# Kernel tuning notes

Hardware: AMD Instinct MI355X
Metric: run time of the kernel (lower is better)

The kernel has to match this reference:

```python
import jax, jax.numpy as jnp
import numpy as np

B, T, I, H, O, R = 128, 1024, 64, 512, 32, 2
TAU = 0.2
NOISE_STD = 0.05


def setup_inputs() -> dict:
    key = jax.random.key(0)
    ks = jax.random.split(key, 12)
    def xavier(k, shape):
        fan_in, fan_out = shape[1], shape[0]
        lim = float(np.sqrt(6.0 / (fan_in + fan_out)))
        return jax.random.uniform(k, shape, jnp.float32, -lim, lim)
    return {
        "u": jax.random.normal(ks[0], (B, T, I), jnp.float32),
        "x0": jax.random.normal(ks[1], (B, H), jnp.float32),
        "noise": jax.random.normal(ks[2], (T, B, H), jnp.float32),
        "Win_w": xavier(ks[3], (H, I)),
        "Win_b": jnp.zeros((H,), jnp.float32),
        "Wout_w": xavier(ks[4], (O, H)),
        "Wout_b": jax.random.normal(ks[5], (O,), jnp.float32) * 0.01,
        "M_rnn": xavier(ks[6], (H, R)),
        "N_rnn": xavier(ks[7], (H, R)),
        "L_tb": xavier(ks[8], (H, R)),
        "M_tb": xavier(ks[9], (H, R)),
        "N_tb": xavier(ks[10], (H, R)),
    }


def reference(u, x0, noise, Win_w, Win_b, Wout_w, Wout_b,
              M_rnn, N_rnn, L_tb, M_tb, N_tb):
    # mode='cont', form='rate', adv=False
    Hdim = x0.shape[1]
    scale_rnn = 1.0 / Hdim
    scale_tb = 1.0 / (Hdim * Hdim)
    # precompute input projection for all timesteps: [T, B, H]
    inp_t = jnp.transpose(jnp.einsum('bti,hi->bth', u, Win_w) + Win_b, (1, 0, 2))

    def step(x, xs):
        ip, nz = xs                                # [B,H] each
        r = jnp.tanh(x)                            # rate form
        rec_rnn = (r @ N_rnn) @ M_rnn.T * scale_rnn
        rec_tb = ((r @ M_tb) * (r @ N_tb)) @ L_tb.T * scale_tb
        rec_x = rec_rnn + rec_tb + ip
        x_new = x + NOISE_STD * nz + TAU * (-x + rec_x)
        return x_new, x_new

    x_final, traj_t = jax.lax.scan(step, x0, (inp_t, noise))
    traj = jnp.transpose(traj_t, (1, 0, 2))        # [B,T,H]
    output = jnp.tanh(traj) @ Wout_w.T + Wout_b    # [B,T,O]
    return output, x_final, traj
```

## Files before the change

### kernel.cpp

```cpp
#include <hip/hip_runtime.h>

constexpr int kB = 128;
constexpr int kT = 1024;
constexpr int kI = 64;
constexpr int kH = 512;
constexpr int kO = 32;
constexpr float kTau = 0.2f;
constexpr float kNoise = 0.05f;

__device__ __forceinline__ float fast_tanh(float x) {
    float e = __expf(2.0f * x);
    return 1.0f - 2.0f * __builtin_amdgcn_rcpf(e + 1.0f);
}

#define BARW() do { asm volatile("s_waitcnt lgkmcnt(0)" ::: "memory"); \
                    __builtin_amdgcn_s_barrier();                      \
                    asm volatile("" ::: "memory"); } while (0)

template <int CTRL, int RMASK>
__device__ __forceinline__ float dpp_add(float s) {
    return s + __int_as_float(__builtin_amdgcn_update_dpp(
        0, __float_as_int(s), CTRL, RMASK, 0xf, true));
}
__device__ __forceinline__ float wave_sum64_lane63(float s) {
    s = dpp_add<0x111, 0xf>(s);
    s = dpp_add<0x112, 0xf>(s);
    s = dpp_add<0x114, 0xf>(s);
    s = dpp_add<0x118, 0xf>(s);
    s = dpp_add<0x142, 0xa>(s);
    s = dpp_add<0x143, 0xc>(s);
    return s;
}

__global__ __launch_bounds__(512, 2) void scan_kernel(
    const float* __restrict__ u, const float* __restrict__ x0,
    const float* __restrict__ noise, const float* __restrict__ Win_w,
    const float* __restrict__ Win_b, const float* __restrict__ M_rnn,
    const float* __restrict__ N_rnn, const float* __restrict__ L_tb,
    const float* __restrict__ M_tb, const float* __restrict__ N_tb,
    float* __restrict__ traj, float* __restrict__ xfin)
{
    const int b    = blockIdx.x;
    const int h    = threadIdx.x;
    const int wid  = h >> 6;
    const int lane = h & 63;

    __shared__ float red[6 * kH];
    __shared__ __align__(16) float res[8];

    float W[kI];
    #pragma unroll
    for (int i = 0; i < kI; i += 4) {
        float4 w = *(const float4*)&Win_w[h * kI + i];
        W[i] = w.x; W[i + 1] = w.y; W[i + 2] = w.z; W[i + 3] = w.w;
    }
    #pragma unroll
    for (int i = 0; i < kI; ++i) asm volatile("" : "+v"(W[i]));

    const float wb  = Win_b[h];
    const float Nr0 = N_rnn[h * 2], Nr1 = N_rnn[h * 2 + 1];
    const float Mt0 = M_tb[h * 2],  Mt1 = M_tb[h * 2 + 1];
    const float Nt0 = N_tb[h * 2],  Nt1 = N_tb[h * 2 + 1];
    const float sc_rnn = 1.0f / (float)kH;
    const float sc_tb  = 1.0f / ((float)kH * (float)kH);
    const float Mr0 = M_rnn[h * 2] * sc_rnn, Mr1 = M_rnn[h * 2 + 1] * sc_rnn;
    const float Lt0 = L_tb[h * 2] * sc_tb,   Lt1 = L_tb[h * 2 + 1] * sc_tb;

    float x = x0[b * kH + h];

    const float* up  = u + (size_t)b * kT * kI;
    const float* nzp = noise + (size_t)b * kH + h;
    float* tp = traj + (size_t)b * kT * kH + h;

    float4 ur[16];
    {
        const float4* u4 = (const float4*)up;
        #pragma unroll
        for (int i = 0; i < 16; ++i) ur[i] = u4[i];
    }
    float nzA = nzp[0];
    float nzB = nzp[(size_t)kB * kH];

    auto step = [&](int t, float& nzC) {
        float r = fast_tanh(x);
        red[0 * kH + h] = r * Nr0;
        red[1 * kH + h] = r * Nr1;
        red[2 * kH + h] = r * Mt0;
        red[3 * kH + h] = r * Mt1;
        red[4 * kH + h] = r * Nt0;
        red[5 * kH + h] = r * Nt1;
        BARW();
        if (wid < 6) {
            const float* c = red + wid * kH + lane;
            float s0 = c[0]   + c[64];
            float s1 = c[128] + c[192];
            float s2 = c[256] + c[320];
            float s3 = c[384] + c[448];
            float s  = (s0 + s1) + (s2 + s3);
            s = wave_sum64_lane63(s);
            if (lane == 63) res[wid] = s;
        }
        BARW();
        float4 r4 = *(const float4*)&res[0];
        float2 r2 = *(const float2*)&res[4];
        float ip = wb;
        #pragma unroll
        for (int i = 0; i < 16; ++i) {
            ip += ur[i].x * W[4 * i]     + ur[i].y * W[4 * i + 1]
                + ur[i].z * W[4 * i + 2] + ur[i].w * W[4 * i + 3];
        }
        {
            int tn = (t + 1 < kT) ? t + 1 : kT - 1;
            const float4* u4 = (const float4*)(up + (size_t)tn * kI);
            #pragma unroll
            for (int i = 0; i < 16; ++i) ur[i] = u4[i];
        }
        float rec = r4.x * Mr0 + r4.y * Mr1
                  + (r4.z * r2.x) * Lt0 + (r4.w * r2.y) * Lt1 + ip;
        x = (1.0f - kTau) * x + kNoise * nzC + kTau * rec;
        tp[(size_t)t * kH] = x;
        int t2 = (t + 2 < kT) ? t + 2 : kT - 1;
        nzC = nzp[(size_t)t2 * kB * kH];
    };

    for (int t = 0; t < kT; t += 2) {
        step(t, nzA);
        step(t + 1, nzB);
    }
    xfin[b * kH + h] = x;
}

constexpr int R_BLK = 256;
constexpr int H_CHK = 32;
constexpr int AS_LD = 260;

__global__ __launch_bounds__(256, 2) void out_kernel(
    const float* __restrict__ traj, const float* __restrict__ Wout_w,
    const float* __restrict__ Wout_b, float* __restrict__ out)
{
    __shared__ float As[H_CHK][AS_LD];
    __shared__ float Ws[H_CHK][36];

    const int tid = threadIdx.x;
    const size_t row0 = (size_t)blockIdx.x * R_BLK;
    const int og = tid & 3;
    const int rg = tid >> 2;

    float acc[4][8];
    #pragma unroll
    for (int k = 0; k < 4; ++k)
        #pragma unroll
        for (int j = 0; j < 8; ++j) acc[k][j] = 0.f;

    const int lr = tid >> 3;
    const int lc4 = tid & 7;
    const int wo = tid >> 3;
    const int wc = (tid & 7) * 4;

    for (int ch = 0; ch < 16; ++ch) {
        const int hc = ch * H_CHK;
        float4 a[8];
        #pragma unroll
        for (int j = 0; j < 8; ++j) {
            const int r = j * 32 + lr;
            a[j] = *(const float4*)&traj[(row0 + r) * kH + hc + lc4 * 4];
        }
        float4 w = *(const float4*)&Wout_w[wo * kH + hc + wc];
        __syncthreads();
        #pragma unroll
        for (int j = 0; j < 8; ++j) {
            const int r = j * 32 + lr;
            As[lc4 * 4 + 0][r] = fast_tanh(a[j].x);
            As[lc4 * 4 + 1][r] = fast_tanh(a[j].y);
            As[lc4 * 4 + 2][r] = fast_tanh(a[j].z);
            As[lc4 * 4 + 3][r] = fast_tanh(a[j].w);
        }
        Ws[wc + 0][wo] = w.x;
        Ws[wc + 1][wo] = w.y;
        Ws[wc + 2][wo] = w.z;
        Ws[wc + 3][wo] = w.w;
        __syncthreads();
        #pragma unroll
        for (int hh = 0; hh < H_CHK; ++hh) {
            float4 av = *(const float4*)&As[hh][rg * 4];
            float4 w0 = *(const float4*)&Ws[hh][og * 8];
            float4 w1 = *(const float4*)&Ws[hh][og * 8 + 4];
            const float av4[4] = {av.x, av.y, av.z, av.w};
            const float wv[8]  = {w0.x, w0.y, w0.z, w0.w,
                                  w1.x, w1.y, w1.z, w1.w};
            #pragma unroll
            for (int k = 0; k < 4; ++k)
                #pragma unroll
                for (int j = 0; j < 8; ++j)
                    acc[k][j] += av4[k] * wv[j];
        }
    }

    #pragma unroll
    for (int k = 0; k < 4; ++k) {
        const size_t row = row0 + rg * 4 + k;
        float4 v0, v1;
        v0.x = acc[k][0] + Wout_b[og * 8 + 0];
        v0.y = acc[k][1] + Wout_b[og * 8 + 1];
        v0.z = acc[k][2] + Wout_b[og * 8 + 2];
        v0.w = acc[k][3] + Wout_b[og * 8 + 3];
        v1.x = acc[k][4] + Wout_b[og * 8 + 4];
        v1.y = acc[k][5] + Wout_b[og * 8 + 5];
        v1.z = acc[k][6] + Wout_b[og * 8 + 6];
        v1.w = acc[k][7] + Wout_b[og * 8 + 7];
        *(float4*)&out[row * kO + og * 8]     = v0;
        *(float4*)&out[row * kO + og * 8 + 4] = v1;
    }
}

extern "C" void kernel_launch(void* const* d_in, const int* in_sizes, int n_in,
                              void* d_out, int out_size, void* d_ws, size_t ws_size,
                              hipStream_t stream) {
    const float* u      = (const float*)d_in[0];
    const float* x0     = (const float*)d_in[1];
    const float* noise  = (const float*)d_in[2];
    const float* Win_w  = (const float*)d_in[3];
    const float* Win_b  = (const float*)d_in[4];
    const float* Wout_w = (const float*)d_in[5];
    const float* Wout_b = (const float*)d_in[6];
    const float* M_rnn  = (const float*)d_in[7];
    const float* N_rnn  = (const float*)d_in[8];
    const float* L_tb   = (const float*)d_in[9];
    const float* M_tb   = (const float*)d_in[10];
    const float* N_tb   = (const float*)d_in[11];

    float* out  = (float*)d_out;
    float* xfin = out + (size_t)kB * kT * kO;
    float* traj = xfin + (size_t)kB * kH;

    scan_kernel<<<dim3(kB), dim3(kH), 0, stream>>>(
        u, x0, noise, Win_w, Win_b, M_rnn, N_rnn, L_tb, M_tb, N_tb, traj, xfin);
    out_kernel<<<dim3((kB * kT) / R_BLK), dim3(256), 0, stream>>>(
        traj, Wout_w, Wout_b, out);
}
```

Measured before the change: 1.466 ms.

## Precompute input projection and noise, shuffle-based scan reduction, double-buffer output GEMM

Adds a separate parallel kernel that computes tau-scaled input projection plus noise for every (b,t) and stores it into the traj buffer. The serial scan then reads that precomputed term in place of the 64-wide dot product and the noise load each step. The scan's cross-thread reduction now uses DPP reductions per wave plus a small shared-memory stage, rather than a 6x512 shared array. The output kernel gains double-buffered LDS with register prefetch and a remapped block order. This adds an extra full pass writing and reading traj in exchange for a shorter serial critical path.

```diff
diff --git a/kernel.cpp b/kernel.cpp
--- a/kernel.cpp
+++ b/kernel.cpp
@@ -22,20 +22,53 @@
     return s + __int_as_float(__builtin_amdgcn_update_dpp(
         0, __float_as_int(s), CTRL, RMASK, 0xf, true));
 }
-__device__ __forceinline__ float wave_sum64_lane63(float s) {
-    s = dpp_add<0x111, 0xf>(s);
-    s = dpp_add<0x112, 0xf>(s);
-    s = dpp_add<0x114, 0xf>(s);
-    s = dpp_add<0x118, 0xf>(s);
-    s = dpp_add<0x142, 0xa>(s);
-    s = dpp_add<0x143, 0xc>(s);
-    return s;
+
+constexpr int ROWS_PB = 64;
+
+__global__ __launch_bounds__(256, 2) void inp_kernel(
+    const float* __restrict__ u, const float* __restrict__ Win_w,
+    const float* __restrict__ Win_b, const float* __restrict__ noise,
+    float* __restrict__ traj)
+{
+    const int tid = threadIdx.x;
+    const int h2 = tid * 2;
+    const size_t row0 = (size_t)blockIdx.x * ROWS_PB;
+
+    float W0[kI], W1[kI];
+    #pragma unroll
+    for (int i = 0; i < kI; i += 4) {
+        float4 a = *(const float4*)&Win_w[(size_t)h2 * kI + i];
+        float4 c = *(const float4*)&Win_w[(size_t)(h2 + 1) * kI + i];
+        W0[i] = a.x * kTau; W0[i + 1] = a.y * kTau;
+        W0[i + 2] = a.z * kTau; W0[i + 3] = a.w * kTau;
+        W1[i] = c.x * kTau; W1[i + 1] = c.y * kTau;
+        W1[i + 2] = c.z * kTau; W1[i + 3] = c.w * kTau;
+    }
+    const float twb0 = Win_b[h2] * kTau;
+    const float twb1 = Win_b[h2 + 1] * kTau;
+
+    for (int r = 0; r < ROWS_PB; ++r) {
+        const size_t row = row0 + r;
+        const float* ur = u + row * kI;
+        float ip0 = twb0, ip1 = twb1;
+        #pragma unroll
+        for (int i = 0; i < kI; ++i) {
+            float ui = ur[i];
+            ip0 += ui * W0[i];
+            ip1 += ui * W1[i];
+        }
+        const int t = (int)(row & (kT - 1));
+        const int b = (int)(row >> 10);
+        float2 nz = *(const float2*)&noise[((size_t)t * kB + b) * kH + h2];
+        float2 c;
+        c.x = ip0 + kNoise * nz.x;
+        c.y = ip1 + kNoise * nz.y;
+        *(float2*)&traj[row * kH + h2] = c;
+    }
 }
 
 __global__ __launch_bounds__(512, 2) void scan_kernel(
-    const float* __restrict__ u, const float* __restrict__ x0,
-    const float* __restrict__ noise, const float* __restrict__ Win_w,
-    const float* __restrict__ Win_b, const float* __restrict__ M_rnn,
+    const float* __restrict__ x0, const float* __restrict__ M_rnn,
     const float* __restrict__ N_rnn, const float* __restrict__ L_tb,
     const float* __restrict__ M_tb, const float* __restrict__ N_tb,
     float* __restrict__ traj, float* __restrict__ xfin)
@@ -45,87 +78,69 @@
     const int wid  = h >> 6;
     const int lane = h & 63;
 
-    __shared__ float red[6 * kH];
+    __shared__ float pp[64];
     __shared__ __align__(16) float res[8];
 
-    float W[kI];
-    #pragma unroll
-    for (int i = 0; i < kI; i += 4) {
-        float4 w = *(const float4*)&Win_w[h * kI + i];
-        W[i] = w.x; W[i + 1] = w.y; W[i + 2] = w.z; W[i + 3] = w.w;
-    }
-    #pragma unroll
-    for (int i = 0; i < kI; ++i) asm volatile("" : "+v"(W[i]));
-
-    const float wb  = Win_b[h];
     const float Nr0 = N_rnn[h * 2], Nr1 = N_rnn[h * 2 + 1];
     const float Mt0 = M_tb[h * 2],  Mt1 = M_tb[h * 2 + 1];
     const float Nt0 = N_tb[h * 2],  Nt1 = N_tb[h * 2 + 1];
-    const float sc_rnn = 1.0f / (float)kH;
-    const float sc_tb  = 1.0f / ((float)kH * (float)kH);
-    const float Mr0 = M_rnn[h * 2] * sc_rnn, Mr1 = M_rnn[h * 2 + 1] * sc_rnn;
-    const float Lt0 = L_tb[h * 2] * sc_tb,   Lt1 = L_tb[h * 2 + 1] * sc_tb;
+    const float sr = kTau / (float)kH;
+    const float st = kTau / ((float)kH * (float)kH);
+    const float tMr0 = M_rnn[h * 2] * sr, tMr1 = M_rnn[h * 2 + 1] * sr;
+    const float tLt0 = L_tb[h * 2] * st,  tLt1 = L_tb[h * 2 + 1] * st;
 
     float x = x0[b * kH + h];
-
-    const float* up  = u + (size_t)b * kT * kI;
-    const float* nzp = noise + (size_t)b * kH + h;
     float* tp = traj + (size_t)b * kT * kH + h;
 
-    float4 ur[16];
-    {
-        const float4* u4 = (const float4*)up;
-        #pragma unroll
-        for (int i = 0; i < 16; ++i) ur[i] = u4[i];
-    }
-    float nzA = nzp[0];
-    float nzB = nzp[(size_t)kB * kH];
-
-    auto step = [&](int t, float& nzC) {
+    float cA = tp[0];
+    float cB = tp[kH];
+
+    auto step = [&](int t, float& c) {
         float r = fast_tanh(x);
-        red[0 * kH + h] = r * Nr0;
-        red[1 * kH + h] = r * Nr1;
-        red[2 * kH + h] = r * Mt0;
-        red[3 * kH + h] = r * Mt1;
-        red[4 * kH + h] = r * Nt0;
-        red[5 * kH + h] = r * Nt1;
-        BARW();
-        if (wid < 6) {
-            const float* c = red + wid * kH + lane;
-            float s0 = c[0]   + c[64];
-            float s1 = c[128] + c[192];
-            float s2 = c[256] + c[320];
-            float s3 = c[384] + c[448];
-            float s  = (s0 + s1) + (s2 + s3);
-            s = wave_sum64_lane63(s);
-            if (lane == 63) res[wid] = s;
+        float s0 = r * Nr0, s1 = r * Nr1;
+        float s2 = r * Mt0, s3 = r * Mt1;
+        float s4 = r * Nt0, s5 = r * Nt1;
+        #define STAGE(CTRL, MASK)                                   \
+            s0 = dpp_add<CTRL, MASK>(s0); s1 = dpp_add<CTRL, MASK>(s1); \
+            s2 = dpp_add<CTRL, MASK>(s2); s3 = dpp_add<CTRL, MASK>(s3); \
+            s4 = dpp_add<CTRL, MASK>(s4); s5 = dpp_add<CTRL, MASK>(s5);
+        STAGE(0x111, 0xf)
+        STAGE(0x112, 0xf)
+        STAGE(0x114, 0xf)
+        STAGE(0x118, 0xf)
+        STAGE(0x142, 0xa)
+        STAGE(0x143, 0xc)
+        #undef STAGE
+        if (lane == 63) {
+            pp[0 * 8 + wid] = s0;
+            pp[1 * 8 + wid] = s1;
+            pp[2 * 8 + wid] = s2;
+            pp[3 * 8 + wid] = s3;
+            pp[4 * 8 + wid] = s4;
+            pp[5 * 8 + wid] = s5;
+        }
+        BARW();
+        if (wid == 0) {
+            float v = pp[lane];
+            v = dpp_add<0x111, 0xf>(v);
+            v = dpp_add<0x112, 0xf>(v);
+            v = dpp_add<0x114, 0xf>(v);
+            if ((lane & 7) == 0 && lane < 48) res[lane >> 3] = v;
         }
         BARW();
         float4 r4 = *(const float4*)&res[0];
         float2 r2 = *(const float2*)&res[4];
-        float ip = wb;
-        #pragma unroll
-        for (int i = 0; i < 16; ++i) {
-            ip += ur[i].x * W[4 * i]     + ur[i].y * W[4 * i + 1]
-                + ur[i].z * W[4 * i + 2] + ur[i].w * W[4 * i + 3];
-        }
-        {
-            int tn = (t + 1 < kT) ? t + 1 : kT - 1;
-            const float4* u4 = (const float4*)(up + (size_t)tn * kI);
-            #pragma unroll
-            for (int i = 0; i < 16; ++i) ur[i] = u4[i];
-        }
-        float rec = r4.x * Mr0 + r4.y * Mr1
-                  + (r4.z * r2.x) * Lt0 + (r4.w * r2.y) * Lt1 + ip;
-        x = (1.0f - kTau) * x + kNoise * nzC + kTau * rec;
+        float rr = r4.x * tMr0 + r4.y * tMr1
+                 + (r4.z * r2.x) * tLt0 + (r4.w * r2.y) * tLt1;
+        x = (1.0f - kTau) * x + rr + c;
         tp[(size_t)t * kH] = x;
-        int t2 = (t + 2 < kT) ? t + 2 : kT - 1;
-        nzC = nzp[(size_t)t2 * kB * kH];
+        int t2 = (t + 2) & (kT - 1);
+        c = tp[(size_t)t2 * kH];
     };
 
     for (int t = 0; t < kT; t += 2) {
-        step(t, nzA);
-        step(t + 1, nzB);
+        step(t, cA);
+        step(t + 1, cB);
     }
     xfin[b * kH + h] = x;
 }
@@ -138,13 +153,18 @@
     const float* __restrict__ traj, const float* __restrict__ Wout_w,
     const float* __restrict__ Wout_b, float* __restrict__ out)
 {
-    __shared__ float As[H_CHK][AS_LD];
-    __shared__ float Ws[H_CHK][36];
+    __shared__ float As[2][H_CHK][AS_LD];
+    __shared__ float Ws[2][H_CHK][36];
 
     const int tid = threadIdx.x;
-    const size_t row0 = (size_t)blockIdx.x * R_BLK;
+    const int g = blockIdx.x;
+    const int l = (g & 7) * 4 + ((g >> 3) & 3) + ((g >> 5) << 5);
+    const size_t row0 = (size_t)l * R_BLK;
+
     const int og = tid & 3;
     const int rg = tid >> 2;
+    const int lr = tid >> 3, lc4 = tid & 7;
+    const int wo = tid >> 3, wc = (tid & 7) * 4;
 
     float acc[4][8];
     #pragma unroll
@@ -152,39 +172,41 @@
         #pragma unroll
         for (int j = 0; j < 8; ++j) acc[k][j] = 0.f;
 
-    const int lr = tid >> 3;
-    const int lc4 = tid & 7;
-    const int wo = tid >> 3;
-    const int wc = (tid & 7) * 4;
+    float4 a[8];
+    float4 w;
+    #pragma unroll
+    for (int j = 0; j < 8; ++j)
+        a[j] = *(const float4*)&traj[(row0 + j * 32 + lr) * kH + lc4 * 4];
+    w = *(const float4*)&Wout_w[(size_t)wo * kH + wc];
 
     for (int ch = 0; ch < 16; ++ch) {
-        const int hc = ch * H_CHK;
-        float4 a[8];
+        const int p = ch & 1;
         #pragma unroll
         for (int j = 0; j < 8; ++j) {
-            const int r = j * 32 + lr;
-            a[j] = *(const float4*)&traj[(row0 + r) * kH + hc + lc4 * 4];
-        }
-        float4 w = *(const float4*)&Wout_w[wo * kH + hc + wc];
-        __syncthreads();
-        #pragma unroll
-        for (int j = 0; j < 8; ++j) {
-            const int r = j * 32 + lr;
-            As[lc4 * 4 + 0][r] = fast_tanh(a[j].x);
-            As[lc4 * 4 + 1][r] = fast_tanh(a[j].y);
-            As[lc4 * 4 + 2][r] = fast_tanh(a[j].z);
-            As[lc4 * 4 + 3][r] = fast_tanh(a[j].w);
-        }
-        Ws[wc + 0][wo] = w.x;
-        Ws[wc + 1][wo] = w.y;
-        Ws[wc + 2][wo] = w.z;
-        Ws[wc + 3][wo] = w.w;
-        __syncthreads();
+            const int rr = j * 32 + lr;
+            As[p][lc4 * 4 + 0][rr] = fast_tanh(a[j].x);
+            As[p][lc4 * 4 + 1][rr] = fast_tanh(a[j].y);
+            As[p][lc4 * 4 + 2][rr] = fast_tanh(a[j].z);
+            As[p][lc4 * 4 + 3][rr] = fast_tanh(a[j].w);
+        }
+        Ws[p][wc + 0][wo] = w.x;
+        Ws[p][wc + 1][wo] = w.y;
+        Ws[p][wc + 2][wo] = w.z;
+        Ws[p][wc + 3][wo] = w.w;
+        BARW();
+        if (ch < 15) {
+            const int hc = (ch + 1) * H_CHK;
+            #pragma unroll
+            for (int j = 0; j < 8; ++j)
+                a[j] = *(const float4*)
+                    &traj[(row0 + j * 32 + lr) * kH + hc + lc4 * 4];
+            w = *(const float4*)&Wout_w[(size_t)wo * kH + hc + wc];
+        }
         #pragma unroll
         for (int hh = 0; hh < H_CHK; ++hh) {
-            float4 av = *(const float4*)&As[hh][rg * 4];
-            float4 w0 = *(const float4*)&Ws[hh][og * 8];
-            float4 w1 = *(const float4*)&Ws[hh][og * 8 + 4];
+            float4 av = *(const float4*)&As[p][hh][rg * 4];
+            float4 w0 = *(const float4*)&Ws[p][hh][og * 8];
+            float4 w1 = *(const float4*)&Ws[p][hh][og * 8 + 4];
             const float av4[4] = {av.x, av.y, av.z, av.w};
             const float wv[8]  = {w0.x, w0.y, w0.z, w0.w,
                                   w1.x, w1.y, w1.z, w1.w};
@@ -194,6 +216,7 @@
                 for (int j = 0; j < 8; ++j)
                     acc[k][j] += av4[k] * wv[j];
         }
+        BARW();
     }
 
     #pragma unroll
@@ -233,8 +256,10 @@
     float* xfin = out + (size_t)kB * kT * kO;
     float* traj = xfin + (size_t)kB * kH;
 
+    inp_kernel<<<dim3((kB * kT) / ROWS_PB), dim3(256), 0, stream>>>(
+        u, Win_w, Win_b, noise, traj);
     scan_kernel<<<dim3(kB), dim3(kH), 0, stream>>>(
-        u, x0, noise, Win_w, Win_b, M_rnn, N_rnn, L_tb, M_tb, N_tb, traj, xfin);
+        x0, M_rnn, N_rnn, L_tb, M_tb, N_tb, traj, xfin);
     out_kernel<<<dim3((kB * kT) / R_BLK), dim3(256), 0, stream>>>(
         traj, Wout_w, Wout_b, out);
 }
```

After: 1.427 ms. -2.7%, faster.
